# Kernel tuning notes

Measured on AMD Instinct MI355X. Metric: run time of the kernel, lower is better.

## Reference

```python
import jax, jax.numpy as jnp
import numpy as np

N = 100000   # num nodes
E = 3200000  # num edges (avg degree 32)
D = 256      # in_channels
H = 256      # hidden_dim
C = 1        # num_class
G = 512      # num graphs in batch


def setup_inputs() -> dict:
    key = jax.random.key(0)
    k = jax.random.split(key, 5)
    x = jax.random.normal(k[0], (N, D), dtype=jnp.float32)
    edge_index = jax.random.randint(k[1], (2, E), 0, N, dtype=jnp.int64)
    batch = jnp.sort(jax.random.randint(k[2], (N,), 0, G, dtype=jnp.int64))
    # GCNLayer.proj: Linear(D, H); model.lin: Linear(H, C)
    W1 = jax.random.normal(k[3], (H, D), dtype=jnp.float32) * 0.05
    b1 = jnp.zeros((H,), dtype=jnp.float32)
    W2 = jax.random.normal(k[4], (C, H), dtype=jnp.float32) * 0.05
    b2 = jnp.zeros((C,), dtype=jnp.float32)
    return {"x": x, "edge_index": edge_index, "batch": batch,
            "W1": W1, "b1": b1, "W2": W2, "b2": b2}


def reference(x, edge_index, batch, W1, b1, W2, b2):
    src, dst = edge_index[0], edge_index[1]
    # degree(edge_index[0]) over ORIGINAL edges (before self-loops), as in source
    deg = jnp.zeros((N,), x.dtype).at[src].add(jnp.asarray(1.0, x.dtype))
    norm = deg ** -0.5  # D^{-1/2}
    # (D^{-1/2} (A + I) D^{-1/2}) x
    # edge term: out[src] += norm[src] * norm[dst] * x[dst]
    msg = (norm[src] * norm[dst])[:, None] * x[dst]          # [E, D]
    agg = jax.ops.segment_sum(msg, src, num_segments=N)      # [N, D]
    agg = agg + (norm * norm)[:, None] * x                   # self-loop term
    h = jax.nn.relu(agg @ W1.T + b1)                          # [N, H]
    pooled = jax.ops.segment_max(h, batch, num_segments=G)   # [G, H]
    out = pooled @ W2.T + b2                                  # [G, 1]
    return jnp.squeeze(out, axis=1)                           # [G]
```

## Files before the change

kernel.cpp:

```cpp
#include <hip/hip_runtime.h>
#include <cstddef>

#define NN    100000
#define EE    3200000
#define GG    512
#define NBKT  1563
#define CAP   2432
#define CBINS 49
#define CCAP  68000
#define TT    4096

typedef __attribute__((ext_vector_type(8))) short bf16x8;
typedef __attribute__((ext_vector_type(4))) float f32x4;
typedef __attribute__((ext_vector_type(8))) unsigned short u16x8;

static __device__ __forceinline__ unsigned short f2b(float f) {
  unsigned u = __float_as_uint(f);
  unsigned r = u + 0x7fffu + ((u >> 16) & 1u);
  return (unsigned short)(r >> 16);
}
static __device__ __forceinline__ float b2f(unsigned short s) {
  return __uint_as_float(((unsigned)s) << 16);
}

__global__ __launch_bounds__(1024, 4) void k_split1(const int* __restrict__ src,
                                                    const int* __restrict__ dst,
                                                    int* __restrict__ ccur,
                                                    int* __restrict__ cpk) {
  __shared__ int hist[CBINS], st[CBINS], cur[CBINS], gbase[CBINS];
  __shared__ int sorted[TT];
  __shared__ unsigned char binof[TT];
  const int tid  = threadIdx.x;
  const int e_lo = blockIdx.x * (EE / 256);
  const int e_hi = e_lo + (EE / 256);

  for (int t0 = e_lo; t0 < e_hi; t0 += TT) {
    const int tc = min(TT, e_hi - t0);
    for (int k = tid; k < CBINS; k += 1024) hist[k] = 0;
    __syncthreads();
    int myk[4], myw[4];
#pragma unroll
    for (int r = 0; r < 4; ++r) {
      int j = r * 1024 + tid;
      myk[r] = -1;
      if (j < tc) {
        int s = src[t0 + j], d = dst[t0 + j];
        myk[r] = s >> 11;
        myw[r] = ((s & 2047) << 17) | d;
        atomicAdd(&hist[myk[r]], 1);
      }
    }
    __syncthreads();
    if (tid < CBINS) {
      int s = 0;
      for (int t = 0; t < tid; ++t) s += hist[t];
      st[tid] = s; cur[tid] = s;
    }
    __syncthreads();
#pragma unroll
    for (int r = 0; r < 4; ++r) {
      if (myk[r] >= 0) {
        int pos = atomicAdd(&cur[myk[r]], 1);
        sorted[pos] = myw[r];
        binof[pos] = (unsigned char)myk[r];
      }
    }
    __syncthreads();
    if (tid < CBINS) {
      int c = cur[tid] - st[tid];
      gbase[tid] = c ? atomicAdd(&ccur[tid], c) : 0;
    }
    __syncthreads();
    for (int j = tid; j < tc; j += 1024) {
      int k = binof[j];
      int idx = gbase[k] + (j - st[k]);
      if (idx < CCAP) cpk[(size_t)k * CCAP + idx] = sorted[j];
    }
    __syncthreads();
  }
}

__global__ __launch_bounds__(1024, 4) void k_split2(const int* __restrict__ ccur,
                                                    const int* __restrict__ cpk,
                                                    int* __restrict__ gcur,
                                                    int* __restrict__ pk) {
  __shared__ int hist[32], st[32], cur[32], gbase[32];
  __shared__ int sorted[TT];
  __shared__ unsigned char binof[TT];
  const int tid  = threadIdx.x;
  const int c    = blockIdx.x >> 4;
  const int sl   = blockIdx.x & 15;
  const int clen = min(ccur[c], CCAP);
  const int lo   = (int)((long long)clen * sl / 16);
  const int hi   = (int)((long long)clen * (sl + 1) / 16);
  const int* __restrict__ cp = cpk + (size_t)c * CCAP;

  for (int t0 = lo; t0 < hi; t0 += TT) {
    const int tc = min(TT, hi - t0);
    if (tid < 32) hist[tid] = 0;
    __syncthreads();
    int myk[4], myw[4];
#pragma unroll
    for (int r = 0; r < 4; ++r) {
      int j = r * 1024 + tid;
      myk[r] = -1;
      if (j < tc) {
        int w    = cp[t0 + j];
        int sl11 = w >> 17;
        myk[r] = sl11 >> 6;
        myw[r] = ((sl11 & 63) << 17) | (w & 0x1FFFF);
        atomicAdd(&hist[myk[r]], 1);
      }
    }
    __syncthreads();
    if (tid < 32) {
      int s = 0;
      for (int t = 0; t < tid; ++t) s += hist[t];
      st[tid] = s; cur[tid] = s;
    }
    __syncthreads();
#pragma unroll
    for (int r = 0; r < 4; ++r) {
      if (myk[r] >= 0) {
        int pos = atomicAdd(&cur[myk[r]], 1);
        sorted[pos] = myw[r];
        binof[pos] = (unsigned char)myk[r];
      }
    }
    __syncthreads();
    if (tid < 32) {
      int cnum = cur[tid] - st[tid];
      gbase[tid] = cnum ? atomicAdd(&gcur[c * 32 + tid], cnum) : 0;
    }
    __syncthreads();
    for (int j = tid; j < tc; j += 1024) {
      int k   = binof[j];
      int idx = gbase[k] + (j - st[k]);
      if (idx < CAP) pk[(size_t)(c * 32 + k) * CAP + idx] = sorted[j];
    }
    __syncthreads();
  }
}

__global__ __launch_bounds__(512) void k_prep(const int* __restrict__ gcur,
                                              const int* __restrict__ pk,
                                              const float* __restrict__ x,
                                              const float* __restrict__ w1,
                                              unsigned short* __restrict__ ybf,
                                              unsigned short* __restrict__ wbf,
                                              int* __restrict__ csr,
                                              int* __restrict__ ro) {
  __shared__ int hist[64], start[65], cur[64];
  const int tid = threadIdx.x;
  const int b   = blockIdx.x;
  const int n0  = b * 64;

  if (tid < 64) hist[tid] = 0;
  __syncthreads();
  const int szc = min(gcur[b], CAP);
  for (int j = tid; j < szc; j += 512)
    atomicAdd(&hist[pk[b * CAP + j] >> 17], 1);
  __syncthreads();
  if (tid < 64) {
    int s = 0;
    for (int t = 0; t < tid; ++t) s += hist[t];
    start[tid] = s; cur[tid] = s;
    if (tid == 63) start[64] = s + hist[63];
  }
  __syncthreads();
  for (int j = tid; j < szc; j += 512) {
    int w = pk[b * CAP + j];
    int pos = atomicAdd(&cur[w >> 17], 1);
    csr[b * CAP + pos] = w & 0x1FFFF;
  }
  if (tid < 65) ro[b * 65 + tid] = start[tid];

  for (int it = 0; it < 8; ++it) {
    int idx = it * 512 + tid;
    int row = idx >> 6, c4 = idx & 63;
    int n = n0 + row;
    if (n < NN) {
      float nr = rsqrtf((float)hist[row]);
      float4 v = ((const float4*)x)[(size_t)n * 64 + c4];
      ushort4 o;
      o.x = f2b(nr * v.x); o.y = f2b(nr * v.y); o.z = f2b(nr * v.z); o.w = f2b(nr * v.w);
      ((ushort4*)ybf)[(size_t)n * 64 + c4] = o;
    }
  }
  if (b < 64 && tid < 256) {
    int i = b * 256 + tid;
    float4 v = ((const float4*)w1)[i];
    ushort4 o;
    o.x = f2b(v.x); o.y = f2b(v.y); o.z = f2b(v.z); o.w = f2b(v.w);
    ((ushort4*)wbf)[i] = o;
  }
}

__global__ __launch_bounds__(512, 8) void k_fused4(const int* __restrict__ ro,
                                                   const int* __restrict__ csr,
                                                   const unsigned short* __restrict__ ybf,
                                                   const unsigned short* __restrict__ wbf,
                                                   const float* __restrict__ b1,
                                                   const int* __restrict__ batch,
                                                   int* __restrict__ pooled) {
  __shared__ __align__(16) unsigned short As[16][264];
  __shared__ int rs[17];
  __shared__ int bg[16];
  const int tid  = threadIdx.x;
  const int n0   = blockIdx.x * 16;
  const int bkt  = blockIdx.x >> 2;
  const int br   = (blockIdx.x & 3) * 16;
  const int wave = tid >> 6;
  const int lane = tid & 63;

  if (tid < 17) rs[tid] = ro[bkt * 65 + br + tid];
  else if (tid >= 64 && tid < 80) bg[tid - 64] = batch[n0 + tid - 64];
  __syncthreads();

  const int half = lane >> 5, l32 = lane & 31;
  const int il   = wave * 2 + half;
  const int i    = n0 + il;
  const u16x8* __restrict__ yr = (const u16x8*)ybf;
  const int* __restrict__ ce = csr + (size_t)bkt * CAP;

  u16x8 sv = yr[(size_t)i * 32 + l32];
  float acc[8];
#pragma unroll
  for (int c = 0; c < 8; ++c) acc[c] = b2f(sv[c]);

  int e = rs[il];
  const int e1 = rs[il + 1];
  const float ni = rsqrtf((float)(e1 - e));
  for (; e + 8 <= e1; e += 8) {
    int d0 = ce[e],     d1 = ce[e + 1], d2 = ce[e + 2], d3 = ce[e + 3];
    int d4 = ce[e + 4], d5 = ce[e + 5], d6 = ce[e + 6], d7 = ce[e + 7];
    u16x8 v0 = yr[(size_t)d0 * 32 + l32];
    u16x8 v1 = yr[(size_t)d1 * 32 + l32];
    u16x8 v2 = yr[(size_t)d2 * 32 + l32];
    u16x8 v3 = yr[(size_t)d3 * 32 + l32];
    u16x8 v4 = yr[(size_t)d4 * 32 + l32];
    u16x8 v5 = yr[(size_t)d5 * 32 + l32];
    u16x8 v6 = yr[(size_t)d6 * 32 + l32];
    u16x8 v7 = yr[(size_t)d7 * 32 + l32];
#pragma unroll
    for (int c = 0; c < 8; ++c)
      acc[c] += ((b2f(v0[c]) + b2f(v1[c])) + (b2f(v2[c]) + b2f(v3[c]))) +
                ((b2f(v4[c]) + b2f(v5[c])) + (b2f(v6[c]) + b2f(v7[c])));
  }
  for (; e + 4 <= e1; e += 4) {
    int d0 = ce[e], d1 = ce[e + 1], d2 = ce[e + 2], d3 = ce[e + 3];
    u16x8 v0 = yr[(size_t)d0 * 32 + l32];
    u16x8 v1 = yr[(size_t)d1 * 32 + l32];
    u16x8 v2 = yr[(size_t)d2 * 32 + l32];
    u16x8 v3 = yr[(size_t)d3 * 32 + l32];
#pragma unroll
    for (int c = 0; c < 8; ++c)
      acc[c] += (b2f(v0[c]) + b2f(v1[c])) + (b2f(v2[c]) + b2f(v3[c]));
  }
  for (; e < e1; ++e) {
    u16x8 v = yr[(size_t)ce[e] * 32 + l32];
#pragma unroll
    for (int c = 0; c < 8; ++c) acc[c] += b2f(v[c]);
  }
  u16x8 o;
#pragma unroll
  for (int c = 0; c < 8; ++c) o[c] = f2b(ni * acc[c]);
  *(u16x8*)&As[il][l32 * 8] = o;
  __syncthreads();

  const int r16 = lane & 15, quad = lane >> 4;
  f32x4 acc4[2];
#pragma unroll
  for (int t = 0; t < 2; ++t) acc4[t] = (f32x4){0.f, 0.f, 0.f, 0.f};
  for (int kc = 0; kc < 8; ++kc) {
    bf16x8 af = *(const bf16x8*)&As[r16][kc * 32 + quad * 8];
#pragma unroll
    for (int ct = 0; ct < 2; ++ct) {
      const int n = wave * 32 + ct * 16 + r16;
      bf16x8 bf = *(const bf16x8*)(wbf + (size_t)n * 256 + kc * 32 + quad * 8);
      acc4[ct] = __builtin_amdgcn_mfma_f32_16x16x32_bf16(af, bf, acc4[ct], 0, 0, 0);
    }
  }

  const int g0 = bg[0], g15 = bg[15];
  if (g0 == g15) {
#pragma unroll
    for (int ct = 0; ct < 2; ++ct) {
      const int col = wave * 32 + ct * 16 + r16;
      const float bias = b1[col];
      float m = 0.f;
#pragma unroll
      for (int r = 0; r < 4; ++r) m = fmaxf(m, acc4[ct][r] + bias);
      m = fmaxf(m, __shfl_xor(m, 16, 64));
      m = fmaxf(m, __shfl_xor(m, 32, 64));
      if (quad == 0) atomicMax(&pooled[g0 * 256 + col], __float_as_int(m));
    }
  } else {
#pragma unroll
    for (int ct = 0; ct < 2; ++ct) {
      const int col = wave * 32 + ct * 16 + r16;
      const float bias = b1[col];
      for (int g = g0; g <= g15; ++g) {
        float m = 0.f;
#pragma unroll
        for (int r = 0; r < 4; ++r) {
          const int row = quad * 4 + r;
          float v = fmaxf(acc4[ct][r] + bias, 0.f);
          if (bg[row] == g) m = fmaxf(m, v);
        }
        m = fmaxf(m, __shfl_xor(m, 16, 64));
        m = fmaxf(m, __shfl_xor(m, 32, 64));
        if (quad == 0) atomicMax(&pooled[g * 256 + col], __float_as_int(m));
      }
    }
  }
}

__global__ void k_out(const float* __restrict__ pooled, const float* __restrict__ w2,
                      const float* __restrict__ b2, float* __restrict__ out) {
  const int wave = threadIdx.x >> 6;
  const int lane = threadIdx.x & 63;
  const int g = blockIdx.x * 4 + wave;
  float4 p = ((const float4*)pooled)[g * 64 + lane];
  float4 w = ((const float4*)w2)[lane];
  float s = p.x * w.x + p.y * w.y + p.z * w.z + p.w * w.w;
  for (int off = 32; off; off >>= 1) s += __shfl_down(s, off, 64);
  if (lane == 0) out[g] = s + b2[0];
}

extern "C" void kernel_launch(void* const* d_in, const int* in_sizes, int n_in,
                              void* d_out, int out_size, void* d_ws, size_t ws_size,
                              hipStream_t stream) {
  const float* x     = (const float*)d_in[0];
  const int*   ei    = (const int*)d_in[1];
  const int*   batch = (const int*)d_in[2];
  const float* W1    = (const float*)d_in[3];
  const float* b1    = (const float*)d_in[4];
  const float* W2    = (const float*)d_in[5];
  const float* b2    = (const float*)d_in[6];
  const int* src = ei;
  const int* dst = ei + EE;
  float* out = (float*)d_out;

  size_t off = 0;
  auto carve = [&](size_t bytes) -> void* {
    void* p = (char*)d_ws + off;
    off += (bytes + 255) & ~(size_t)255;
    return p;
  };
  int*   pooled = (int*)carve((size_t)GG * 256 * 4);
  int*   gcur   = (int*)carve((size_t)NBKT * 4);
  int*   ccur   = (int*)carve((size_t)CBINS * 4);
  const size_t zlen = off;
  unsigned short* ybf = (unsigned short*)carve((size_t)NN * 256 * 2);
  int*   cpk    = (int*)carve((size_t)CBINS * CCAP * 4);
  int*   pk     = (int*)carve((size_t)NBKT * CAP * 4);
  int*   csr    = (int*)carve((size_t)NBKT * CAP * 4);
  int*   ro     = (int*)carve((size_t)NBKT * 65 * 4);
  unsigned short* wbf = (unsigned short*)carve(256 * 256 * 2);

  hipMemsetAsync(pooled, 0, zlen, stream);

  k_split1<<<256,        1024, 0, stream>>>(src, dst, ccur, cpk);
  k_split2<<<CBINS * 16, 1024, 0, stream>>>(ccur, cpk, gcur, pk);
  k_prep  <<<NBKT,        512, 0, stream>>>(gcur, pk, x, W1, ybf, wbf, csr, ro);
  k_fused4<<<NN / 16,     512, 0, stream>>>(ro, csr, ybf, wbf, b1, batch, pooled);
  k_out   <<<GG / 4,      256, 0, stream>>>((const float*)pooled, W2, b2, out);
}
```

Measured before the change: 468.9 us.

## Split fused gather+GEMM into feature-sliced gather kernel and separate MFMA kernel

```diff
diff --git a/kernel.cpp b/kernel.cpp
--- a/kernel.cpp
+++ b/kernel.cpp
@@ -9,6 +9,8 @@
 #define CBINS 49
 #define CCAP  68000
 #define TT    4096
+#define NSL   16
+#define SLB   1568
 
 typedef __attribute__((ext_vector_type(8))) short bf16x8;
 typedef __attribute__((ext_vector_type(4))) float f32x4;
@@ -146,7 +148,7 @@
                                               const int* __restrict__ pk,
                                               const float* __restrict__ x,
                                               const float* __restrict__ w1,
-                                              unsigned short* __restrict__ ybf,
+                                              unsigned short* __restrict__ ysl,
                                               unsigned short* __restrict__ wbf,
                                               int* __restrict__ csr,
                                               int* __restrict__ ro) {
@@ -184,7 +186,7 @@
       float4 v = ((const float4*)x)[(size_t)n * 64 + c4];
       ushort4 o;
       o.x = f2b(nr * v.x); o.y = f2b(nr * v.y); o.z = f2b(nr * v.z); o.w = f2b(nr * v.w);
-      ((ushort4*)ybf)[(size_t)n * 64 + c4] = o;
+      ((ushort4*)ysl)[((size_t)(c4 >> 2) * NN + n) * 4 + (c4 & 3)] = o;
     }
   }
   if (b < 64 && tid < 256) {
@@ -196,89 +198,86 @@
   }
 }
 
-__global__ __launch_bounds__(512, 8) void k_fused4(const int* __restrict__ ro,
-                                                   const int* __restrict__ csr,
-                                                   const unsigned short* __restrict__ ybf,
-                                                   const unsigned short* __restrict__ wbf,
-                                                   const float* __restrict__ b1,
-                                                   const int* __restrict__ batch,
-                                                   int* __restrict__ pooled) {
-  __shared__ __align__(16) unsigned short As[16][264];
-  __shared__ int rs[17];
+__global__ __launch_bounds__(128, 8) void k_gath(const int* __restrict__ ro,
+                                                 const int* __restrict__ csr,
+                                                 const unsigned short* __restrict__ ysl,
+                                                 unsigned short* __restrict__ agg) {
+  __shared__ int cl[CAP];
+  __shared__ int rs[65];
+  const int sb = blockIdx.x;
+  const int s  = sb / SLB;
+  const int b  = sb - s * SLB;
+  if (b >= NBKT) return;
+  const int tid = threadIdx.x;
+  const int total = ro[b * 65 + 64];
+  if (tid < 65) rs[tid] = ro[b * 65 + tid];
+  for (int j = tid; j < total; j += 128) cl[j] = csr[(size_t)b * CAP + j];
+  __syncthreads();
+
+  const int r = tid >> 1, half = tid & 1;
+  const int n = b * 64 + r;
+  if (n >= NN) return;
+  const size_t sbase = (size_t)s * NN;
+  const u16x8* __restrict__ Y = (const u16x8*)ysl;
+
+  const int e0 = rs[r], e1 = rs[r + 1];
+  const float ni = rsqrtf((float)(e1 - e0));
+  u16x8 sv = Y[(sbase + n) * 2 + half];
+  float acc[8];
+#pragma unroll
+  for (int c = 0; c < 8; ++c) acc[c] = b2f(sv[c]);
+
+  int e = e0;
+  for (; e + 4 <= e1; e += 4) {
+    int d0 = cl[e], d1 = cl[e + 1], d2 = cl[e + 2], d3 = cl[e + 3];
+    u16x8 v0 = Y[(sbase + d0) * 2 + half];
+    u16x8 v1 = Y[(sbase + d1) * 2 + half];
+    u16x8 v2 = Y[(sbase + d2) * 2 + half];
+    u16x8 v3 = Y[(sbase + d3) * 2 + half];
+#pragma unroll
+    for (int c = 0; c < 8; ++c)
+      acc[c] += (b2f(v0[c]) + b2f(v1[c])) + (b2f(v2[c]) + b2f(v3[c]));
+  }
+  for (; e < e1; ++e) {
+    u16x8 v = Y[(sbase + cl[e]) * 2 + half];
+#pragma unroll
+    for (int c = 0; c < 8; ++c) acc[c] += b2f(v[c]);
+  }
+  u16x8 o;
+#pragma unroll
+  for (int c = 0; c < 8; ++c) o[c] = f2b(ni * acc[c]);
+  __builtin_nontemporal_store(o, (u16x8*)agg + ((size_t)n * 32 + s * 2 + half));
+}
+
+__global__ __launch_bounds__(512, 4) void k_mm(const unsigned short* __restrict__ agg,
+                                               const unsigned short* __restrict__ wbf,
+                                               const float* __restrict__ b1,
+                                               const int* __restrict__ batch,
+                                               int* __restrict__ pooled) {
   __shared__ int bg[16];
   const int tid  = threadIdx.x;
   const int n0   = blockIdx.x * 16;
-  const int bkt  = blockIdx.x >> 2;
-  const int br   = (blockIdx.x & 3) * 16;
   const int wave = tid >> 6;
   const int lane = tid & 63;
-
-  if (tid < 17) rs[tid] = ro[bkt * 65 + br + tid];
-  else if (tid >= 64 && tid < 80) bg[tid - 64] = batch[n0 + tid - 64];
-  __syncthreads();
-
-  const int half = lane >> 5, l32 = lane & 31;
-  const int il   = wave * 2 + half;
-  const int i    = n0 + il;
-  const u16x8* __restrict__ yr = (const u16x8*)ybf;
-  const int* __restrict__ ce = csr + (size_t)bkt * CAP;
-
-  u16x8 sv = yr[(size_t)i * 32 + l32];
-  float acc[8];
-#pragma unroll
-  for (int c = 0; c < 8; ++c) acc[c] = b2f(sv[c]);
-
-  int e = rs[il];
-  const int e1 = rs[il + 1];
-  const float ni = rsqrtf((float)(e1 - e));
-  for (; e + 8 <= e1; e += 8) {
-    int d0 = ce[e],     d1 = ce[e + 1], d2 = ce[e + 2], d3 = ce[e + 3];
-    int d4 = ce[e + 4], d5 = ce[e + 5], d6 = ce[e + 6], d7 = ce[e + 7];
-    u16x8 v0 = yr[(size_t)d0 * 32 + l32];
-    u16x8 v1 = yr[(size_t)d1 * 32 + l32];
-    u16x8 v2 = yr[(size_t)d2 * 32 + l32];
-    u16x8 v3 = yr[(size_t)d3 * 32 + l32];
-    u16x8 v4 = yr[(size_t)d4 * 32 + l32];
-    u16x8 v5 = yr[(size_t)d5 * 32 + l32];
-    u16x8 v6 = yr[(size_t)d6 * 32 + l32];
-    u16x8 v7 = yr[(size_t)d7 * 32 + l32];
-#pragma unroll
-    for (int c = 0; c < 8; ++c)
-      acc[c] += ((b2f(v0[c]) + b2f(v1[c])) + (b2f(v2[c]) + b2f(v3[c]))) +
-                ((b2f(v4[c]) + b2f(v5[c])) + (b2f(v6[c]) + b2f(v7[c])));
-  }
-  for (; e + 4 <= e1; e += 4) {
-    int d0 = ce[e], d1 = ce[e + 1], d2 = ce[e + 2], d3 = ce[e + 3];
-    u16x8 v0 = yr[(size_t)d0 * 32 + l32];
-    u16x8 v1 = yr[(size_t)d1 * 32 + l32];
-    u16x8 v2 = yr[(size_t)d2 * 32 + l32];
-    u16x8 v3 = yr[(size_t)d3 * 32 + l32];
-#pragma unroll
-    for (int c = 0; c < 8; ++c)
-      acc[c] += (b2f(v0[c]) + b2f(v1[c])) + (b2f(v2[c]) + b2f(v3[c]));
-  }
-  for (; e < e1; ++e) {
-    u16x8 v = yr[(size_t)ce[e] * 32 + l32];
-#pragma unroll
-    for (int c = 0; c < 8; ++c) acc[c] += b2f(v[c]);
-  }
-  u16x8 o;
-#pragma unroll
-  for (int c = 0; c < 8; ++c) o[c] = f2b(ni * acc[c]);
-  *(u16x8*)&As[il][l32 * 8] = o;
+  if (tid < 16) bg[tid] = batch[n0 + tid];
   __syncthreads();
 
   const int r16 = lane & 15, quad = lane >> 4;
+  bf16x8 af[8];
+#pragma unroll
+  for (int kc = 0; kc < 8; ++kc)
+    af[kc] = *(const bf16x8*)(agg + (size_t)(n0 + r16) * 256 + kc * 32 + quad * 8);
+
   f32x4 acc4[2];
 #pragma unroll
   for (int t = 0; t < 2; ++t) acc4[t] = (f32x4){0.f, 0.f, 0.f, 0.f};
+#pragma unroll
   for (int kc = 0; kc < 8; ++kc) {
-    bf16x8 af = *(const bf16x8*)&As[r16][kc * 32 + quad * 8];
 #pragma unroll
     for (int ct = 0; ct < 2; ++ct) {
-      const int n = wave * 32 + ct * 16 + r16;
-      bf16x8 bf = *(const bf16x8*)(wbf + (size_t)n * 256 + kc * 32 + quad * 8);
-      acc4[ct] = __builtin_amdgcn_mfma_f32_16x16x32_bf16(af, bf, acc4[ct], 0, 0, 0);
+      const int nw = wave * 32 + ct * 16 + r16;
+      bf16x8 bf = *(const bf16x8*)(wbf + (size_t)nw * 256 + kc * 32 + quad * 8);
+      acc4[ct] = __builtin_amdgcn_mfma_f32_16x16x32_bf16(af[kc], bf, acc4[ct], 0, 0, 0);
     }
   }
 
@@ -352,18 +351,20 @@
   int*   gcur   = (int*)carve((size_t)NBKT * 4);
   int*   ccur   = (int*)carve((size_t)CBINS * 4);
   const size_t zlen = off;
-  unsigned short* ybf = (unsigned short*)carve((size_t)NN * 256 * 2);
+  unsigned short* ysl = (unsigned short*)carve((size_t)NN * 256 * 2);
   int*   cpk    = (int*)carve((size_t)CBINS * CCAP * 4);
   int*   pk     = (int*)carve((size_t)NBKT * CAP * 4);
   int*   csr    = (int*)carve((size_t)NBKT * CAP * 4);
   int*   ro     = (int*)carve((size_t)NBKT * 65 * 4);
   unsigned short* wbf = (unsigned short*)carve(256 * 256 * 2);
+  unsigned short* agg = (unsigned short*)carve((size_t)NN * 256 * 2);
 
   hipMemsetAsync(pooled, 0, zlen, stream);
 
   k_split1<<<256,        1024, 0, stream>>>(src, dst, ccur, cpk);
   k_split2<<<CBINS * 16, 1024, 0, stream>>>(ccur, cpk, gcur, pk);
-  k_prep  <<<NBKT,        512, 0, stream>>>(gcur, pk, x, W1, ybf, wbf, csr, ro);
-  k_fused4<<<NN / 16,     512, 0, stream>>>(ro, csr, ybf, wbf, b1, batch, pooled);
+  k_prep  <<<NBKT,        512, 0, stream>>>(gcur, pk, x, W1, ysl, wbf, csr, ro);
+  k_gath  <<<NSL * SLB,   128, 0, stream>>>(ro, csr, ysl, agg);
+  k_mm    <<<NN / 16,     512, 0, stream>>>(agg, wbf, b1, batch, pooled);
   k_out   <<<GG / 4,      256, 0, stream>>>((const float*)pooled, W2, b2, out);
 }
```

Result: slower. 716.9 us (+52.9%).

## Use one wave per node in fused gather and stage CSR indices in LDS

Applied to the files above, without the earlier changes.

```diff
diff --git a/kernel.cpp b/kernel.cpp
--- a/kernel.cpp
+++ b/kernel.cpp
@@ -22,6 +22,8 @@
 static __device__ __forceinline__ float b2f(unsigned short s) {
   return __uint_as_float(((unsigned)s) << 16);
 }
+#define BL(v) b2f((unsigned short)(v))
+#define BH(v) b2f((unsigned short)((v) >> 16))
 
 __global__ __launch_bounds__(1024, 4) void k_split1(const int* __restrict__ src,
                                                     const int* __restrict__ dst,
@@ -196,14 +198,15 @@
   }
 }
 
-__global__ __launch_bounds__(512, 8) void k_fused4(const int* __restrict__ ro,
-                                                   const int* __restrict__ csr,
-                                                   const unsigned short* __restrict__ ybf,
-                                                   const unsigned short* __restrict__ wbf,
-                                                   const float* __restrict__ b1,
-                                                   const int* __restrict__ batch,
-                                                   int* __restrict__ pooled) {
+__global__ __launch_bounds__(1024, 8) void k_fused4(const int* __restrict__ ro,
+                                                    const int* __restrict__ csr,
+                                                    const unsigned short* __restrict__ ybf,
+                                                    const unsigned short* __restrict__ wbf,
+                                                    const float* __restrict__ b1,
+                                                    const int* __restrict__ batch,
+                                                    int* __restrict__ pooled) {
   __shared__ __align__(16) unsigned short As[16][264];
+  __shared__ int cl[CAP];
   __shared__ int rs[17];
   __shared__ int bg[16];
   const int tid  = threadIdx.x;
@@ -216,102 +219,93 @@
   if (tid < 17) rs[tid] = ro[bkt * 65 + br + tid];
   else if (tid >= 64 && tid < 80) bg[tid - 64] = batch[n0 + tid - 64];
   __syncthreads();
-
-  const int half = lane >> 5, l32 = lane & 31;
-  const int il   = wave * 2 + half;
-  const int i    = n0 + il;
-  const u16x8* __restrict__ yr = (const u16x8*)ybf;
-  const int* __restrict__ ce = csr + (size_t)bkt * CAP;
-
-  u16x8 sv = yr[(size_t)i * 32 + l32];
-  float acc[8];
-#pragma unroll
-  for (int c = 0; c < 8; ++c) acc[c] = b2f(sv[c]);
-
-  int e = rs[il];
-  const int e1 = rs[il + 1];
-  const float ni = rsqrtf((float)(e1 - e));
-  for (; e + 8 <= e1; e += 8) {
-    int d0 = ce[e],     d1 = ce[e + 1], d2 = ce[e + 2], d3 = ce[e + 3];
-    int d4 = ce[e + 4], d5 = ce[e + 5], d6 = ce[e + 6], d7 = ce[e + 7];
-    u16x8 v0 = yr[(size_t)d0 * 32 + l32];
-    u16x8 v1 = yr[(size_t)d1 * 32 + l32];
-    u16x8 v2 = yr[(size_t)d2 * 32 + l32];
-    u16x8 v3 = yr[(size_t)d3 * 32 + l32];
-    u16x8 v4 = yr[(size_t)d4 * 32 + l32];
-    u16x8 v5 = yr[(size_t)d5 * 32 + l32];
-    u16x8 v6 = yr[(size_t)d6 * 32 + l32];
-    u16x8 v7 = yr[(size_t)d7 * 32 + l32];
-#pragma unroll
-    for (int c = 0; c < 8; ++c)
-      acc[c] += ((b2f(v0[c]) + b2f(v1[c])) + (b2f(v2[c]) + b2f(v3[c]))) +
-                ((b2f(v4[c]) + b2f(v5[c])) + (b2f(v6[c]) + b2f(v7[c])));
-  }
-  for (; e + 4 <= e1; e += 4) {
-    int d0 = ce[e], d1 = ce[e + 1], d2 = ce[e + 2], d3 = ce[e + 3];
-    u16x8 v0 = yr[(size_t)d0 * 32 + l32];
-    u16x8 v1 = yr[(size_t)d1 * 32 + l32];
-    u16x8 v2 = yr[(size_t)d2 * 32 + l32];
-    u16x8 v3 = yr[(size_t)d3 * 32 + l32];
-#pragma unroll
-    for (int c = 0; c < 8; ++c)
-      acc[c] += (b2f(v0[c]) + b2f(v1[c])) + (b2f(v2[c]) + b2f(v3[c]));
-  }
-  for (; e < e1; ++e) {
-    u16x8 v = yr[(size_t)ce[e] * 32 + l32];
-#pragma unroll
-    for (int c = 0; c < 8; ++c) acc[c] += b2f(v[c]);
-  }
-  u16x8 o;
-#pragma unroll
-  for (int c = 0; c < 8; ++c) o[c] = f2b(ni * acc[c]);
-  *(u16x8*)&As[il][l32 * 8] = o;
+  const int rs0 = rs[0];
+  const int tot = rs[16] - rs0;
+  const int* __restrict__ ce = csr + (size_t)bkt * CAP + rs0;
+  for (int j = tid; j < tot; j += 1024) cl[j] = ce[j];
+  __syncthreads();
+
+  const int il = wave;
+  const int i  = n0 + il;
+  const uint2* __restrict__ yr = (const uint2*)ybf;
+
+  int eb       = rs[il] - rs0;
+  const int ee = rs[il + 1] - rs0;
+  const float ni = rsqrtf((float)(ee - eb));
+  uint2 sv = yr[(size_t)i * 64 + lane];
+  float a0 = BL(sv.x), a1 = BH(sv.x), a2 = BL(sv.y), a3 = BH(sv.y);
+
+  for (; eb + 8 <= ee; eb += 8) {
+    int d0 = cl[eb],     d1 = cl[eb + 1], d2 = cl[eb + 2], d3 = cl[eb + 3];
+    int d4 = cl[eb + 4], d5 = cl[eb + 5], d6 = cl[eb + 6], d7 = cl[eb + 7];
+    uint2 v0 = yr[(size_t)d0 * 64 + lane];
+    uint2 v1 = yr[(size_t)d1 * 64 + lane];
+    uint2 v2 = yr[(size_t)d2 * 64 + lane];
+    uint2 v3 = yr[(size_t)d3 * 64 + lane];
+    uint2 v4 = yr[(size_t)d4 * 64 + lane];
+    uint2 v5 = yr[(size_t)d5 * 64 + lane];
+    uint2 v6 = yr[(size_t)d6 * 64 + lane];
+    uint2 v7 = yr[(size_t)d7 * 64 + lane];
+    a0 += ((BL(v0.x) + BL(v1.x)) + (BL(v2.x) + BL(v3.x))) +
+          ((BL(v4.x) + BL(v5.x)) + (BL(v6.x) + BL(v7.x)));
+    a1 += ((BH(v0.x) + BH(v1.x)) + (BH(v2.x) + BH(v3.x))) +
+          ((BH(v4.x) + BH(v5.x)) + (BH(v6.x) + BH(v7.x)));
+    a2 += ((BL(v0.y) + BL(v1.y)) + (BL(v2.y) + BL(v3.y))) +
+          ((BL(v4.y) + BL(v5.y)) + (BL(v6.y) + BL(v7.y)));
+    a3 += ((BH(v0.y) + BH(v1.y)) + (BH(v2.y) + BH(v3.y))) +
+          ((BH(v4.y) + BH(v5.y)) + (BH(v6.y) + BH(v7.y)));
+  }
+  for (; eb + 4 <= ee; eb += 4) {
+    int d0 = cl[eb], d1 = cl[eb + 1], d2 = cl[eb + 2], d3 = cl[eb + 3];
+    uint2 v0 = yr[(size_t)d0 * 64 + lane];
+    uint2 v1 = yr[(size_t)d1 * 64 + lane];
+    uint2 v2 = yr[(size_t)d2 * 64 + lane];
+    uint2 v3 = yr[(size_t)d3 * 64 + lane];
+    a0 += (BL(v0.x) + BL(v1.x)) + (BL(v2.x) + BL(v3.x));
+    a1 += (BH(v0.x) + BH(v1.x)) + (BH(v2.x) + BH(v3.x));
+    a2 += (BL(v0.y) + BL(v1.y)) + (BL(v2.y) + BL(v3.y));
+    a3 += (BH(v0.y) + BH(v1.y)) + (BH(v2.y) + BH(v3.y));
+  }
+  for (; eb < ee; ++eb) {
+    uint2 v = yr[(size_t)cl[eb] * 64 + lane];
+    a0 += BL(v.x); a1 += BH(v.x); a2 += BL(v.y); a3 += BH(v.y);
+  }
+  ushort4 o;
+  o.x = f2b(ni * a0); o.y = f2b(ni * a1); o.z = f2b(ni * a2); o.w = f2b(ni * a3);
+  *(ushort4*)&As[il][lane * 4] = o;
   __syncthreads();
 
   const int r16 = lane & 15, quad = lane >> 4;
-  f32x4 acc4[2];
-#pragma unroll
-  for (int t = 0; t < 2; ++t) acc4[t] = (f32x4){0.f, 0.f, 0.f, 0.f};
+  f32x4 acc4 = (f32x4){0.f, 0.f, 0.f, 0.f};
   for (int kc = 0; kc < 8; ++kc) {
     bf16x8 af = *(const bf16x8*)&As[r16][kc * 32 + quad * 8];
-#pragma unroll
-    for (int ct = 0; ct < 2; ++ct) {
-      const int n = wave * 32 + ct * 16 + r16;
-      bf16x8 bf = *(const bf16x8*)(wbf + (size_t)n * 256 + kc * 32 + quad * 8);
-      acc4[ct] = __builtin_amdgcn_mfma_f32_16x16x32_bf16(af, bf, acc4[ct], 0, 0, 0);
-    }
+    const int n = wave * 16 + r16;
+    bf16x8 bf = *(const bf16x8*)(wbf + (size_t)n * 256 + kc * 32 + quad * 8);
+    acc4 = __builtin_amdgcn_mfma_f32_16x16x32_bf16(af, bf, acc4, 0, 0, 0);
   }
 
   const int g0 = bg[0], g15 = bg[15];
+  const int col = wave * 16 + r16;
+  const float bias = b1[col];
   if (g0 == g15) {
-#pragma unroll
-    for (int ct = 0; ct < 2; ++ct) {
-      const int col = wave * 32 + ct * 16 + r16;
-      const float bias = b1[col];
+    float m = 0.f;
+#pragma unroll
+    for (int r = 0; r < 4; ++r) m = fmaxf(m, acc4[r] + bias);
+    m = fmaxf(m, __shfl_xor(m, 16, 64));
+    m = fmaxf(m, __shfl_xor(m, 32, 64));
+    if (quad == 0) atomicMax(&pooled[g0 * 256 + col], __float_as_int(m));
+  } else {
+    for (int g = g0; g <= g15; ++g) {
       float m = 0.f;
 #pragma unroll
-      for (int r = 0; r < 4; ++r) m = fmaxf(m, acc4[ct][r] + bias);
+      for (int r = 0; r < 4; ++r) {
+        const int row = quad * 4 + r;
+        float v = fmaxf(acc4[r] + bias, 0.f);
+        if (bg[row] == g) m = fmaxf(m, v);
+      }
       m = fmaxf(m, __shfl_xor(m, 16, 64));
       m = fmaxf(m, __shfl_xor(m, 32, 64));
-      if (quad == 0) atomicMax(&pooled[g0 * 256 + col], __float_as_int(m));
-    }
-  } else {
-#pragma unroll
-    for (int ct = 0; ct < 2; ++ct) {
-      const int col = wave * 32 + ct * 16 + r16;
-      const float bias = b1[col];
-      for (int g = g0; g <= g15; ++g) {
-        float m = 0.f;
-#pragma unroll
-        for (int r = 0; r < 4; ++r) {
-          const int row = quad * 4 + r;
-          float v = fmaxf(acc4[ct][r] + bias, 0.f);
-          if (bg[row] == g) m = fmaxf(m, v);
-        }
-        m = fmaxf(m, __shfl_xor(m, 16, 64));
-        m = fmaxf(m, __shfl_xor(m, 32, 64));
-        if (quad == 0) atomicMax(&pooled[g * 256 + col], __float_as_int(m));
-      }
+      if (quad == 0) atomicMax(&pooled[g * 256 + col], __float_as_int(m));
     }
   }
 }
@@ -364,6 +358,6 @@
   k_split1<<<256,        1024, 0, stream>>>(src, dst, ccur, cpk);
   k_split2<<<CBINS * 16, 1024, 0, stream>>>(ccur, cpk, gcur, pk);
   k_prep  <<<NBKT,        512, 0, stream>>>(gcur, pk, x, W1, ybf, wbf, csr, ro);
-  k_fused4<<<NN / 16,     512, 0, stream>>>(ro, csr, ybf, wbf, b1, batch, pooled);
+  k_fused4<<<NN / 16,    1024, 0, stream>>>(ro, csr, ybf, wbf, b1, batch, pooled);
   k_out   <<<GG / 4,      256, 0, stream>>>((const float*)pooled, W2, b2, out);
 }
```

Result: slower. 488.6 us (+4.2%).

## Collapse two-pass edge bucketing into single pass with 256-node buckets

Applied to the files above, without the earlier changes.

```diff
diff --git a/kernel.cpp b/kernel.cpp
--- a/kernel.cpp
+++ b/kernel.cpp
@@ -4,10 +4,8 @@
 #define NN    100000
 #define EE    3200000
 #define GG    512
-#define NBKT  1563
-#define CAP   2432
-#define CBINS 49
-#define CCAP  68000
+#define NBK2  391
+#define BCAP  9216
 #define TT    4096
 
 typedef __attribute__((ext_vector_type(8))) short bf16x8;
@@ -23,20 +21,21 @@
   return __uint_as_float(((unsigned)s) << 16);
 }
 
-__global__ __launch_bounds__(1024, 4) void k_split1(const int* __restrict__ src,
-                                                    const int* __restrict__ dst,
-                                                    int* __restrict__ ccur,
-                                                    int* __restrict__ cpk) {
-  __shared__ int hist[CBINS], st[CBINS], cur[CBINS], gbase[CBINS];
+__global__ __launch_bounds__(1024, 2) void k_split(const int* __restrict__ src,
+                                                   const int* __restrict__ dst,
+                                                   int* __restrict__ gcur,
+                                                   int* __restrict__ pk) {
+  __shared__ int hist[NBK2], st[NBK2], cur[NBK2], gbase[NBK2];
+  __shared__ int sc[512];
   __shared__ int sorted[TT];
-  __shared__ unsigned char binof[TT];
+  __shared__ unsigned short binof[TT];
   const int tid  = threadIdx.x;
   const int e_lo = blockIdx.x * (EE / 256);
   const int e_hi = e_lo + (EE / 256);
 
   for (int t0 = e_lo; t0 < e_hi; t0 += TT) {
     const int tc = min(TT, e_hi - t0);
-    for (int k = tid; k < CBINS; k += 1024) hist[k] = 0;
+    if (tid < NBK2) hist[tid] = 0;
     __syncthreads();
     int myk[4], myw[4];
 #pragma unroll
@@ -45,98 +44,40 @@
       myk[r] = -1;
       if (j < tc) {
         int s = src[t0 + j], d = dst[t0 + j];
-        myk[r] = s >> 11;
-        myw[r] = ((s & 2047) << 17) | d;
+        myk[r] = s >> 8;
+        myw[r] = ((s & 255) << 17) | d;
         atomicAdd(&hist[myk[r]], 1);
       }
     }
     __syncthreads();
-    if (tid < CBINS) {
-      int s = 0;
-      for (int t = 0; t < tid; ++t) s += hist[t];
-      st[tid] = s; cur[tid] = s;
-    }
+    if (tid < 512) sc[tid] = (tid < NBK2) ? hist[tid] : 0;
+    __syncthreads();
+    for (int d = 1; d < 512; d <<= 1) {
+      int v = (tid < 512 && tid >= d) ? sc[tid - d] : 0;
+      __syncthreads();
+      if (tid < 512) sc[tid] += v;
+      __syncthreads();
+    }
+    if (tid < NBK2) { st[tid] = tid ? sc[tid - 1] : 0; cur[tid] = st[tid]; }
     __syncthreads();
 #pragma unroll
     for (int r = 0; r < 4; ++r) {
       if (myk[r] >= 0) {
         int pos = atomicAdd(&cur[myk[r]], 1);
         sorted[pos] = myw[r];
-        binof[pos] = (unsigned char)myk[r];
+        binof[pos] = (unsigned short)myk[r];
       }
     }
     __syncthreads();
-    if (tid < CBINS) {
+    if (tid < NBK2) {
       int c = cur[tid] - st[tid];
-      gbase[tid] = c ? atomicAdd(&ccur[tid], c) : 0;
-    }
-    __syncthreads();
-    for (int j = tid; j < tc; j += 1024) {
-      int k = binof[j];
-      int idx = gbase[k] + (j - st[k]);
-      if (idx < CCAP) cpk[(size_t)k * CCAP + idx] = sorted[j];
-    }
-    __syncthreads();
-  }
-}
-
-__global__ __launch_bounds__(1024, 4) void k_split2(const int* __restrict__ ccur,
-                                                    const int* __restrict__ cpk,
-                                                    int* __restrict__ gcur,
-                                                    int* __restrict__ pk) {
-  __shared__ int hist[32], st[32], cur[32], gbase[32];
-  __shared__ int sorted[TT];
-  __shared__ unsigned char binof[TT];
-  const int tid  = threadIdx.x;
-  const int c    = blockIdx.x >> 4;
-  const int sl   = blockIdx.x & 15;
-  const int clen = min(ccur[c], CCAP);
-  const int lo   = (int)((long long)clen * sl / 16);
-  const int hi   = (int)((long long)clen * (sl + 1) / 16);
-  const int* __restrict__ cp = cpk + (size_t)c * CCAP;
-
-  for (int t0 = lo; t0 < hi; t0 += TT) {
-    const int tc = min(TT, hi - t0);
-    if (tid < 32) hist[tid] = 0;
-    __syncthreads();
-    int myk[4], myw[4];
-#pragma unroll
-    for (int r = 0; r < 4; ++r) {
-      int j = r * 1024 + tid;
-      myk[r] = -1;
-      if (j < tc) {
-        int w    = cp[t0 + j];
-        int sl11 = w >> 17;
-        myk[r] = sl11 >> 6;
-        myw[r] = ((sl11 & 63) << 17) | (w & 0x1FFFF);
-        atomicAdd(&hist[myk[r]], 1);
-      }
-    }
-    __syncthreads();
-    if (tid < 32) {
-      int s = 0;
-      for (int t = 0; t < tid; ++t) s += hist[t];
-      st[tid] = s; cur[tid] = s;
-    }
-    __syncthreads();
-#pragma unroll
-    for (int r = 0; r < 4; ++r) {
-      if (myk[r] >= 0) {
-        int pos = atomicAdd(&cur[myk[r]], 1);
-        sorted[pos] = myw[r];
-        binof[pos] = (unsigned char)myk[r];
-      }
-    }
-    __syncthreads();
-    if (tid < 32) {
-      int cnum = cur[tid] - st[tid];
-      gbase[tid] = cnum ? atomicAdd(&gcur[c * 32 + tid], cnum) : 0;
+      gbase[tid] = c ? atomicAdd(&gcur[tid], c) : 0;
     }
     __syncthreads();
     for (int j = tid; j < tc; j += 1024) {
       int k   = binof[j];
       int idx = gbase[k] + (j - st[k]);
-      if (idx < CAP) pk[(size_t)(c * 32 + k) * CAP + idx] = sorted[j];
+      if (idx < BCAP) pk[(size_t)k * BCAP + idx] = sorted[j];
     }
     __syncthreads();
   }
@@ -150,37 +91,44 @@
                                               unsigned short* __restrict__ wbf,
                                               int* __restrict__ csr,
                                               int* __restrict__ ro) {
-  __shared__ int hist[64], start[65], cur[64];
+  __shared__ int hist[256], start[257], cur[256], sc[256];
   const int tid = threadIdx.x;
   const int b   = blockIdx.x;
-  const int n0  = b * 64;
-
-  if (tid < 64) hist[tid] = 0;
-  __syncthreads();
-  const int szc = min(gcur[b], CAP);
+  const int n0  = b * 256;
+
+  if (tid < 256) hist[tid] = 0;
+  __syncthreads();
+  const int szc = min(gcur[b], BCAP);
+  const int* __restrict__ pb = pk + (size_t)b * BCAP;
   for (int j = tid; j < szc; j += 512)
-    atomicAdd(&hist[pk[b * CAP + j] >> 17], 1);
-  __syncthreads();
-  if (tid < 64) {
-    int s = 0;
-    for (int t = 0; t < tid; ++t) s += hist[t];
-    start[tid] = s; cur[tid] = s;
-    if (tid == 63) start[64] = s + hist[63];
-  }
+    atomicAdd(&hist[pb[j] >> 17], 1);
+  __syncthreads();
+  if (tid < 256) sc[tid] = hist[tid];
+  __syncthreads();
+  for (int d = 1; d < 256; d <<= 1) {
+    int v = (tid < 256 && tid >= d) ? sc[tid - d] : 0;
+    __syncthreads();
+    if (tid < 256) sc[tid] += v;
+    __syncthreads();
+  }
+  if (tid < 256) { start[tid] = tid ? sc[tid - 1] : 0; cur[tid] = start[tid]; }
+  if (tid == 0) start[256] = 0;
+  __syncthreads();
+  if (tid == 0) start[256] = sc[255];
   __syncthreads();
   for (int j = tid; j < szc; j += 512) {
-    int w = pk[b * CAP + j];
+    int w = pb[j];
     int pos = atomicAdd(&cur[w >> 17], 1);
-    csr[b * CAP + pos] = w & 0x1FFFF;
-  }
-  if (tid < 65) ro[b * 65 + tid] = start[tid];
-
-  for (int it = 0; it < 8; ++it) {
+    csr[(size_t)b * BCAP + pos] = w & 0x1FFFF;
+  }
+  if (tid < 257) ro[b * 257 + tid] = start[tid];
+
+  for (int it = 0; it < 32; ++it) {
     int idx = it * 512 + tid;
     int row = idx >> 6, c4 = idx & 63;
     int n = n0 + row;
     if (n < NN) {
-      float nr = rsqrtf((float)hist[row]);
+      float nr = rsqrtf((float)(start[row + 1] - start[row]));
       float4 v = ((const float4*)x)[(size_t)n * 64 + c4];
       ushort4 o;
       o.x = f2b(nr * v.x); o.y = f2b(nr * v.y); o.z = f2b(nr * v.z); o.w = f2b(nr * v.w);
@@ -208,12 +156,12 @@
   __shared__ int bg[16];
   const int tid  = threadIdx.x;
   const int n0   = blockIdx.x * 16;
-  const int bkt  = blockIdx.x >> 2;
-  const int br   = (blockIdx.x & 3) * 16;
+  const int bkt  = blockIdx.x >> 4;
+  const int br   = (blockIdx.x & 15) * 16;
   const int wave = tid >> 6;
   const int lane = tid & 63;
 
-  if (tid < 17) rs[tid] = ro[bkt * 65 + br + tid];
+  if (tid < 17) rs[tid] = ro[bkt * 257 + br + tid];
   else if (tid >= 64 && tid < 80) bg[tid - 64] = batch[n0 + tid - 64];
   __syncthreads();
 
@@ -221,7 +169,7 @@
   const int il   = wave * 2 + half;
   const int i    = n0 + il;
   const u16x8* __restrict__ yr = (const u16x8*)ybf;
-  const int* __restrict__ ce = csr + (size_t)bkt * CAP;
+  const int* __restrict__ ce = csr + (size_t)bkt * BCAP;
 
   u16x8 sv = yr[(size_t)i * 32 + l32];
   float acc[8];
@@ -349,21 +297,18 @@
     return p;
   };
   int*   pooled = (int*)carve((size_t)GG * 256 * 4);
-  int*   gcur   = (int*)carve((size_t)NBKT * 4);
-  int*   ccur   = (int*)carve((size_t)CBINS * 4);
+  int*   gcur   = (int*)carve((size_t)NBK2 * 4);
   const size_t zlen = off;
   unsigned short* ybf = (unsigned short*)carve((size_t)NN * 256 * 2);
-  int*   cpk    = (int*)carve((size_t)CBINS * CCAP * 4);
-  int*   pk     = (int*)carve((size_t)NBKT * CAP * 4);
-  int*   csr    = (int*)carve((size_t)NBKT * CAP * 4);
-  int*   ro     = (int*)carve((size_t)NBKT * 65 * 4);
+  int*   pk     = (int*)carve((size_t)NBK2 * BCAP * 4);
+  int*   csr    = (int*)carve((size_t)NBK2 * BCAP * 4);
+  int*   ro     = (int*)carve((size_t)NBK2 * 257 * 4);
   unsigned short* wbf = (unsigned short*)carve(256 * 256 * 2);
 
   hipMemsetAsync(pooled, 0, zlen, stream);
 
-  k_split1<<<256,        1024, 0, stream>>>(src, dst, ccur, cpk);
-  k_split2<<<CBINS * 16, 1024, 0, stream>>>(ccur, cpk, gcur, pk);
-  k_prep  <<<NBKT,        512, 0, stream>>>(gcur, pk, x, W1, ybf, wbf, csr, ro);
-  k_fused4<<<NN / 16,     512, 0, stream>>>(ro, csr, ybf, wbf, b1, batch, pooled);
-  k_out   <<<GG / 4,      256, 0, stream>>>((const float*)pooled, W2, b2, out);
-}
+  k_split<<<256,     1024, 0, stream>>>(src, dst, gcur, pk);
+  k_prep <<<NBK2,     512, 0, stream>>>(gcur, pk, x, W1, ybf, wbf, csr, ro);
+  k_fused4<<<NN / 16, 512, 0, stream>>>(ro, csr, ybf, wbf, b1, batch, pooled);
+  k_out  <<<GG / 4,   256, 0, stream>>>((const float*)pooled, W2, b2, out);
+}
```

New measurement: 465.8 us. About the same (-0.7%).
